# Optimization experiments

Measured on AMD Instinct MI355X. Metric: run time of the kernel, lower is better.

## Reference

```python
import jax, jax.numpy as jnp
import numpy as np

N, H, L, O = 8192, 512, 3, 512
LN_EPS = 1e-5


def setup_inputs() -> dict:
    key = jax.random.key(0)
    ks = jax.random.split(key, 8)
    # sparse symmetric adjacency with positive weights, zero diagonal
    u = jax.random.uniform(ks[0], (N, N))
    w = jax.random.uniform(ks[1], (N, N)) * 0.9 + 0.1
    A = jnp.where(u < 0.004, w, 0.0)
    A = (A + A.T) * 0.5
    A = A * (1.0 - jnp.eye(N, dtype=A.dtype))
    s = 0.02
    return {
        "node_feat": jax.random.normal(ks[2], (1, N, H), jnp.float32),
        "adj": A[None],
        "conv_w": jax.random.normal(ks[3], (L, H, H), jnp.float32) * s,
        "conv_b": jnp.zeros((L, H), jnp.float32),
        "mlp_w": jax.random.normal(ks[4], (L, H, H), jnp.float32) * s,
        "mlp_b": jnp.zeros((L, H), jnp.float32),
        "ln_g": jnp.ones((L, H), jnp.float32),
        "ln_b": jnp.zeros((L, H), jnp.float32),
        "lin_w": jax.random.normal(ks[5], (H, O), jnp.float32) * s,
        "lin_b": jnp.zeros((O,), jnp.float32),
    }


def _layer_norm(x, g, b):
    mu = jnp.mean(x, axis=-1, keepdims=True)
    var = jnp.mean(jnp.square(x - mu), axis=-1, keepdims=True)
    return (x - mu) * jax.lax.rsqrt(var + LN_EPS) * g + b


def reference(node_feat, adj, conv_w, conv_b, mlp_w, mlp_b, ln_g, ln_b, lin_w, lin_b):
    x = node_feat[0]          # [N, H]
    A = adj[0]                # [N, N]
    A = jnp.where(A > 0, A, 0.0)  # edges are positive entries only
    # gcn_norm: add self-loops (weight 1) only where missing
    d = jnp.diagonal(A)
    A1 = A + jnp.diag(jnp.where(d > 0, 0.0, 1.0))
    # deg scattered at target (edge_index[1] = column)
    deg = jnp.sum(A1, axis=0)
    dinv = jnp.where(deg > 0, deg ** -0.5, 0.0)
    Ahat = dinv[:, None] * A1 * dinv[None, :]  # [N, N]
    for l in range(L):
        # GCNConv: linear, propagate (aggregate at col), bias
        x = Ahat.T @ (x @ conv_w[l]) + conv_b[l]
        # MLP: Linear -> LayerNorm -> ReLU
        x = jax.nn.relu(_layer_norm(x @ mlp_w[l] + mlp_b[l], ln_g[l], ln_b[l]))
    mu = (x @ lin_w + lin_b)[None]  # [1, N, O]
    return mu
```

## Files before the change

### kernel.cpp

```cpp
#include <hip/hip_runtime.h>

#define NN 8192
#define HD 512
#define NL 3
#define CAPQ 48
#define CAPR (4 * CAPQ)
#define NWB (273 * NL)
#define NSB 2048
#define LN_EPS 1e-5f

typedef _Float16 f16;
typedef _Float16 f16x8 __attribute__((ext_vector_type(8)));
typedef _Float16 f16x4 __attribute__((ext_vector_type(4)));
typedef _Float16 f16x2 __attribute__((ext_vector_type(2)));
typedef float f32x4 __attribute__((ext_vector_type(4)));

__device__ __forceinline__ unsigned short f16_bits(f16 h) {
  union { f16 h; unsigned short u; } x; x.h = h; return x.u;
}
__device__ __forceinline__ f16 bits_f16(unsigned short u) {
  union { unsigned short u; f16 h; } x; x.u = u; return x.h;
}

__global__ __launch_bounds__(256) void k_prep(const float* __restrict__ A,
                                              const float* __restrict__ convw,
                                              const float* __restrict__ mlpw,
                                              const float* __restrict__ convb,
                                              const float* __restrict__ mlpb,
                                              const float* __restrict__ lw,
                                              unsigned* __restrict__ ell,
                                              int* __restrict__ nnz8q,
                                              float* __restrict__ psum,
                                              f16* __restrict__ WlT,
                                              float* __restrict__ bl,
                                              f16* __restrict__ lwT) {
  const int b = blockIdx.x;
  const int t = threadIdx.x;

  if (b < NWB) {
    const int l = b / 273;
    const int bx = b % 273;
    if (bx < 256) {
      const int m0 = bx * 2;
      const float* Wc = convw + (size_t)l * HD * HD;
      const float* Wm = mlpw + (size_t)l * HD * HD;
      f16* o = WlT + (size_t)l * HD * HD;
      float a00 = 0.f, a01 = 0.f, a10 = 0.f, a11 = 0.f;
      const float* wc0 = Wc + (size_t)m0 * HD;
      const float* wc1 = Wc + (size_t)(m0 + 1) * HD;
      for (int k = 0; k < HD; k++) {
        const float w0 = Wm[(size_t)k * HD + t];
        const float w1 = Wm[(size_t)k * HD + t + 256];
        const float c0 = wc0[k];
        const float c1 = wc1[k];
        a00 = fmaf(c0, w0, a00);
        a01 = fmaf(c0, w1, a01);
        a10 = fmaf(c1, w0, a10);
        a11 = fmaf(c1, w1, a11);
      }
      o[(size_t)t * HD + m0] = (f16)a00;
      o[(size_t)(t + 256) * HD + m0] = (f16)a01;
      o[(size_t)t * HD + m0 + 1] = (f16)a10;
      o[(size_t)(t + 256) * HD + m0 + 1] = (f16)a11;
    } else if (bx == 256) {
      const float* Wm = mlpw + (size_t)l * HD * HD;
      float acc0 = mlpb[l * HD + t];
      float acc1 = mlpb[l * HD + t + 256];
      for (int k = 0; k < HD; k++) {
        const float cb = convb[l * HD + k];
        acc0 = fmaf(cb, Wm[(size_t)k * HD + t], acc0);
        acc1 = fmaf(cb, Wm[(size_t)k * HD + t + 256], acc1);
      }
      bl[l * HD + t] = acc0;
      bl[l * HD + t + 256] = acc1;
    } else if (l == 0) {
      const int base = (bx - 257) * 16384;
      #pragma unroll 4
      for (int j = 0; j < 64; j++) {
        const int idx = base + j * 256 + t;
        const int k = idx >> 9, n = idx & 511;
        lwT[(size_t)n * HD + k] = (f16)lw[idx];
      }
    }
    return;
  }

  const int lane = t & 63;
  const int wid = (b - NWB) * 4 + (t >> 6);

  auto LOADQ = [&](int qidx, float4* v) {
    const int r = qidx >> 2, seg = qidx & 3;
    const float4* aseg = (const float4*)(A + (size_t)r * NN + seg * 2048);
    #pragma unroll
    for (int i = 0; i < 8; i++) v[i] = aseg[lane + i * 64];
  };

  auto PROC = [&](int qidx, const float4* v) {
    const int r = qidx >> 2, seg = qidx & 3;
    unsigned* er = ell + (size_t)qidx * CAPQ;
    int c = 0;
    float s = 0.f;
    #pragma unroll
    for (int i = 0; i < 8; i++) {
      c += (v[i].x > 0.f) + (v[i].y > 0.f) + (v[i].z > 0.f) + (v[i].w > 0.f);
      s += v[i].x + v[i].y + v[i].z + v[i].w;
    }
    int inc = c;
    #pragma unroll
    for (int d = 1; d < 64; d <<= 1) {
      int vv = __shfl_up(inc, d);
      if (lane >= d) inc += vv;
    }
    float ss = s;
    #pragma unroll
    for (int m = 1; m < 64; m <<= 1) ss += __shfl_xor(ss, m);
    int o = inc - c;
    #pragma unroll
    for (int i = 0; i < 8; i++) {
      const int cb = seg * 2048 + (lane + i * 64) * 4;
      float vals[4] = {v[i].x, v[i].y, v[i].z, v[i].w};
      #pragma unroll
      for (int q = 0; q < 4; q++) {
        if (vals[q] > 0.f) {
          if (o < CAPQ) er[o] = ((unsigned)f16_bits((f16)vals[q]) << 16) | (unsigned)(cb + q);
          o++;
        }
      }
    }
    int ne = __shfl(inc, 63);
    if (lane == 0) {
      if (ne > CAPQ) ne = CAPQ;
      const bool own = (seg == (r >> 11));
      if (own && ne < CAPQ) { er[ne] = (0x3C00u << 16) | (unsigned)r; ne++; }
      const int n8 = (ne + 7) & ~7;
      for (int k = ne; k < n8; k++) er[k] = (unsigned)r;
      nnz8q[qidx] = n8;
      psum[qidx] = ss;
    }
  };

  float4 va[8], vb[8];
  LOADQ(wid, va);
  LOADQ(wid + 8192, vb);
  PROC(wid, va);
  LOADQ(wid + 16384, va);
  PROC(wid + 8192, vb);
  LOADQ(wid + 24576, vb);
  PROC(wid + 16384, va);
  PROC(wid + 24576, vb);
}

__global__ __launch_bounds__(256) void k_deg(const float* __restrict__ psum,
                                             const float* __restrict__ x0,
                                             float* __restrict__ dinv,
                                             f16* __restrict__ xs) {
  const int r = blockIdx.x * 4 + (threadIdx.x >> 6);
  const int lane = threadIdx.x & 63;
  const float4 ps = *(const float4*)(psum + (size_t)r * 4);
  const float di = rsqrtf(ps.x + ps.y + ps.z + ps.w + 1.f);
  if (lane == 0) dinv[r] = di;
  const float4* xr = (const float4*)(x0 + (size_t)r * HD);
  const float4 a = xr[lane * 2];
  const float4 bq = xr[lane * 2 + 1];
  f16x8 o = {(f16)(a.x * di), (f16)(a.y * di), (f16)(a.z * di), (f16)(a.w * di),
             (f16)(bq.x * di), (f16)(bq.y * di), (f16)(bq.z * di), (f16)(bq.w * di)};
  *(f16x8*)(xs + (size_t)r * HD + lane * 8) = o;
}

__global__ __launch_bounds__(256) void k_spmm(const unsigned* __restrict__ ell,
                                              const int* __restrict__ nnz8q,
                                              const float* __restrict__ dinv,
                                              const f16* __restrict__ xs,
                                              f16* __restrict__ y) {
  const int bid = blockIdx.x;
  const int chunk = bid & 3;
  const int rb = bid >> 2;
  const int r = __builtin_amdgcn_readfirstlane(rb * 4 + (threadIdx.x >> 6));
  const int lane = threadIdx.x & 63;
  const int c0 = chunk * 128 + lane * 2;
  const unsigned* erow = ell + (size_t)r * CAPR;
  const int4 nn = *(const int4*)(nnz8q + (size_t)r * 4);
  const int ne8s[4] = {nn.x >> 3, nn.y >> 3, nn.z >> 3, nn.w >> 3};
  const f16* xc = xs + c0;
  float a0 = 0.f, a1 = 0.f;
  #pragma unroll
  for (int seg = 0; seg < 4; seg++) {
    const uint4* er = (const uint4*)(erow + seg * CAPQ);
    const int ne8 = ne8s[seg];
    for (int e8 = 0; e8 < ne8; e8++) {
      const uint4 ea = er[e8 * 2];
      const uint4 eb = er[e8 * 2 + 1];
      unsigned wv[8] = {ea.x, ea.y, ea.z, ea.w, eb.x, eb.y, eb.z, eb.w};
      f16x2 xv[8];
      #pragma unroll
      for (int q = 0; q < 8; q++)
        xv[q] = *(const f16x2*)(xc + (size_t)(wv[q] & 0xFFFFu) * HD);
      #pragma unroll
      for (int q = 0; q < 8; q++) {
        const float fw = (float)bits_f16((unsigned short)(wv[q] >> 16));
        a0 = fmaf(fw, (float)xv[q][0], a0);
        a1 = fmaf(fw, (float)xv[q][1], a1);
      }
    }
  }
  const float s = dinv[r];
  f16x2 o = {(f16)(a0 * s), (f16)(a1 * s)};
  *(f16x2*)(y + (size_t)r * HD + c0) = o;
}

__global__ __launch_bounds__(512) void k_gemm_ln(const f16* __restrict__ y,
                                                 const f16* __restrict__ WT,
                                                 const float* __restrict__ bias,
                                                 const float* __restrict__ g,
                                                 const float* __restrict__ bb,
                                                 const float* __restrict__ dscale,
                                                 f16* __restrict__ outp) {
  __shared__ float red[32][4][2];
  const int t = threadIdx.x;
  const int lane = t & 63;
  const int w = t >> 6;
  const int wm = w >> 2;
  const int wn = w & 3;
  const int m0 = blockIdx.x * 32;
  const int rl = lane & 15, kg = (lane >> 4) * 8;
  const f16* aP = y + (size_t)(m0 + wm * 16 + rl) * HD + kg;
  const f16* bP = WT + (size_t)(wn * 128 + rl) * HD + kg;

  f32x4 acc[8];
  #pragma unroll
  for (int j = 0; j < 8; j++) { f32x4 z = {0.f, 0.f, 0.f, 0.f}; acc[j] = z; }

  #pragma unroll 2
  for (int ks = 0; ks < HD; ks += 32) {
    const f16x8 af = *(const f16x8*)(aP + ks);
    #pragma unroll
    for (int j = 0; j < 8; j++) {
      const f16x8 bf = *(const f16x8*)(bP + (size_t)j * 16 * HD + ks);
      acc[j] = __builtin_amdgcn_mfma_f32_16x16x32_f16(af, bf, acc[j], 0, 0, 0);
    }
  }

  const int cg = lane >> 4, cl = lane & 15;
  float av[8][4];
  #pragma unroll
  for (int j = 0; j < 8; j++) {
    const float bv = bias[wn * 128 + j * 16 + cl];
    #pragma unroll
    for (int r = 0; r < 4; r++) av[j][r] = acc[j][r] + bv;
  }
  #pragma unroll
  for (int r = 0; r < 4; r++) {
    float s = 0.f, sq = 0.f;
    #pragma unroll
    for (int j = 0; j < 8; j++) { s += av[j][r]; sq += av[j][r] * av[j][r]; }
    #pragma unroll
    for (int m = 1; m < 16; m <<= 1) { s += __shfl_xor(s, m); sq += __shfl_xor(sq, m); }
    if (cl == 0) {
      red[wm * 16 + cg * 4 + r][wn][0] = s;
      red[wm * 16 + cg * 4 + r][wn][1] = sq;
    }
  }
  __syncthreads();
  #pragma unroll
  for (int r = 0; r < 4; r++) {
    const int rb = wm * 16 + cg * 4 + r;
    float s = 0.f, sq = 0.f;
    #pragma unroll
    for (int q = 0; q < 4; q++) { s += red[rb][q][0]; sq += red[rb][q][1]; }
    const float mu = s * (1.f / HD);
    const float rs = rsqrtf(sq * (1.f / HD) - mu * mu + LN_EPS);
    const int row = m0 + rb;
    const float dsc = dscale ? dscale[row] : 1.f;
    #pragma unroll
    for (int j = 0; j < 8; j++) {
      const int col = wn * 128 + j * 16 + cl;
      const float val = fmaxf((av[j][r] - mu) * rs * g[col] + bb[col], 0.f) * dsc;
      outp[(size_t)row * HD + col] = (f16)val;
    }
  }
}

__global__ __launch_bounds__(256) void k_gemm_direct(const f16* __restrict__ A,
                                                     const f16* __restrict__ BT,
                                                     float* __restrict__ C,
                                                     const float* __restrict__ bias) {
  const int t = threadIdx.x;
  const int lane = t & 63;
  const int wave = t >> 6;
  const int wm = wave >> 1, wn = wave & 1;
  const int m0 = blockIdx.x * 128, n0 = blockIdx.y * 128;
  const int rl = lane & 15, kg = (lane >> 4) * 8;

  const f16* aP[4];
  const f16* bP[4];
  #pragma unroll
  for (int i = 0; i < 4; i++)
    aP[i] = A + (size_t)(m0 + wm * 64 + i * 16 + rl) * HD + kg;
  #pragma unroll
  for (int j = 0; j < 4; j++)
    bP[j] = BT + (size_t)(n0 + wn * 64 + j * 16 + rl) * HD + kg;

  f32x4 acc[4][4];
  #pragma unroll
  for (int i = 0; i < 4; i++)
    #pragma unroll
    for (int j = 0; j < 4; j++) {
      f32x4 z = {0.f, 0.f, 0.f, 0.f};
      acc[i][j] = z;
    }

  #pragma unroll 4
  for (int ks = 0; ks < HD; ks += 32) {
    f16x8 af[4], bf[4];
    #pragma unroll
    for (int i = 0; i < 4; i++) af[i] = *(const f16x8*)(aP[i] + ks);
    #pragma unroll
    for (int j = 0; j < 4; j++) bf[j] = *(const f16x8*)(bP[j] + ks);
    #pragma unroll
    for (int i = 0; i < 4; i++)
      #pragma unroll
      for (int j = 0; j < 4; j++)
        acc[i][j] = __builtin_amdgcn_mfma_f32_16x16x32_f16(af[i], bf[j], acc[i][j], 0, 0, 0);
  }

  const int cg = lane >> 4, cl = lane & 15;
  #pragma unroll
  for (int i = 0; i < 4; i++) {
    #pragma unroll
    for (int j = 0; j < 4; j++) {
      const int col = n0 + wn * 64 + j * 16 + cl;
      const float bv = bias ? bias[col] : 0.f;
      #pragma unroll
      for (int rr = 0; rr < 4; rr++) {
        const int row = m0 + wm * 64 + i * 16 + cg * 4 + rr;
        C[(size_t)row * HD + col] = acc[i][j][rr] + bv;
      }
    }
  }
}

extern "C" void kernel_launch(void* const* d_in, const int* in_sizes, int n_in,
                              void* d_out, int out_size, void* d_ws, size_t ws_size,
                              hipStream_t stream) {
  const float* node_feat = (const float*)d_in[0];
  const float* adj       = (const float*)d_in[1];
  const float* conv_w    = (const float*)d_in[2];
  const float* conv_b    = (const float*)d_in[3];
  const float* mlp_w     = (const float*)d_in[4];
  const float* mlp_b     = (const float*)d_in[5];
  const float* ln_g      = (const float*)d_in[6];
  const float* ln_b      = (const float*)d_in[7];
  const float* lin_w     = (const float*)d_in[8];
  const float* lin_b     = (const float*)d_in[9];
  float* out = (float*)d_out;

  char* p = (char*)d_ws;
  unsigned* ell = (unsigned*)p; p += (size_t)NN * CAPR * 4;
  int* nnz8q = (int*)p;  p += (size_t)NN * 4 * 4;
  float* psum = (float*)p; p += (size_t)NN * 4 * 4;
  float* dinv = (float*)p; p += (size_t)NN * 4;
  f16* xsA   = (f16*)p;   p += (size_t)NN * HD * 2;
  f16* xsB   = (f16*)p;   p += (size_t)NN * HD * 2;
  f16* ybuf  = (f16*)p;   p += (size_t)NN * HD * 2;
  f16* WlT   = (f16*)p;   p += (size_t)NL * HD * HD * 2;
  f16* lwT   = (f16*)p;   p += (size_t)HD * HD * 2;
  float* bl  = (float*)p; p += (size_t)NL * HD * 4;

  k_prep<<<NWB + NSB, 256, 0, stream>>>(adj, conv_w, mlp_w, conv_b, mlp_b,
                                        lin_w, ell, nnz8q, psum, WlT, bl, lwT);
  k_deg<<<NN / 4, 256, 0, stream>>>(psum, node_feat, dinv, xsA);

  f16* xcur = xsA;
  for (int l = 0; l < NL; l++) {
    k_spmm<<<NN, 256, 0, stream>>>(ell, nnz8q, dinv, xcur, ybuf);
    f16* nxt = (xcur == xsA) ? xsB : xsA;
    k_gemm_ln<<<NN / 32, 512, 0, stream>>>(ybuf, WlT + (size_t)l * HD * HD,
                                           bl + l * HD, ln_g + l * HD, ln_b + l * HD,
                                           (l < 2) ? dinv : nullptr, nxt);
    xcur = nxt;
  }
  k_gemm_direct<<<dim3(64, 4), 256, 0, stream>>>(xcur, lwT, out, lin_b);
}
```

Before: 330.7 us.

## Stage ELL segments in LDS and write coalesced, one quarter-row per wave

The adjacency-to-ELL conversion now gives each wave exactly one quarter-row segment, launching many more blocks instead of looping four segments per wave with register double-buffering. Nonzeros are compacted into a shared-memory stage buffer pre-filled with the padding index and then written to global memory with one coalesced store per lane, replacing scattered per-element global writes and the serial padding loop. The per-segment capacity rises from 48 to 64 so each lane stores exactly one slot, which writes more ELL bytes and gives up the explicit load/process overlap in exchange for simpler, coalesced stores.

```diff
diff --git a/kernel.cpp b/kernel.cpp
--- a/kernel.cpp
+++ b/kernel.cpp
@@ -3,10 +3,9 @@
 #define NN 8192
 #define HD 512
 #define NL 3
-#define CAPQ 48
+#define CAPQ 64
 #define CAPR (4 * CAPQ)
 #define NWB (273 * NL)
-#define NSB 2048
 #define LN_EPS 1e-5f
 
 typedef _Float16 f16;
@@ -85,69 +84,60 @@
     return;
   }
 
+  __shared__ unsigned stage[4][CAPQ];
   const int lane = t & 63;
-  const int wid = (b - NWB) * 4 + (t >> 6);
-
-  auto LOADQ = [&](int qidx, float4* v) {
-    const int r = qidx >> 2, seg = qidx & 3;
-    const float4* aseg = (const float4*)(A + (size_t)r * NN + seg * 2048);
-    #pragma unroll
-    for (int i = 0; i < 8; i++) v[i] = aseg[lane + i * 64];
-  };
-
-  auto PROC = [&](int qidx, const float4* v) {
-    const int r = qidx >> 2, seg = qidx & 3;
-    unsigned* er = ell + (size_t)qidx * CAPQ;
-    int c = 0;
-    float s = 0.f;
-    #pragma unroll
-    for (int i = 0; i < 8; i++) {
-      c += (v[i].x > 0.f) + (v[i].y > 0.f) + (v[i].z > 0.f) + (v[i].w > 0.f);
-      s += v[i].x + v[i].y + v[i].z + v[i].w;
-    }
-    int inc = c;
-    #pragma unroll
-    for (int d = 1; d < 64; d <<= 1) {
-      int vv = __shfl_up(inc, d);
-      if (lane >= d) inc += vv;
-    }
-    float ss = s;
-    #pragma unroll
-    for (int m = 1; m < 64; m <<= 1) ss += __shfl_xor(ss, m);
-    int o = inc - c;
-    #pragma unroll
-    for (int i = 0; i < 8; i++) {
-      const int cb = seg * 2048 + (lane + i * 64) * 4;
-      float vals[4] = {v[i].x, v[i].y, v[i].z, v[i].w};
-      #pragma unroll
-      for (int q = 0; q < 4; q++) {
-        if (vals[q] > 0.f) {
-          if (o < CAPQ) er[o] = ((unsigned)f16_bits((f16)vals[q]) << 16) | (unsigned)(cb + q);
-          o++;
-        }
-      }
-    }
-    int ne = __shfl(inc, 63);
-    if (lane == 0) {
-      if (ne > CAPQ) ne = CAPQ;
-      const bool own = (seg == (r >> 11));
-      if (own && ne < CAPQ) { er[ne] = (0x3C00u << 16) | (unsigned)r; ne++; }
-      const int n8 = (ne + 7) & ~7;
-      for (int k = ne; k < n8; k++) er[k] = (unsigned)r;
-      nnz8q[qidx] = n8;
-      psum[qidx] = ss;
-    }
-  };
-
-  float4 va[8], vb[8];
-  LOADQ(wid, va);
-  LOADQ(wid + 8192, vb);
-  PROC(wid, va);
-  LOADQ(wid + 16384, va);
-  PROC(wid + 8192, vb);
-  LOADQ(wid + 24576, vb);
-  PROC(wid + 16384, va);
-  PROC(wid + 24576, vb);
+  const int w = t >> 6;
+  const int qidx = (b - NWB) * 4 + w;
+  const int r = qidx >> 2, seg = qidx & 3;
+  const float4* aseg = (const float4*)(A + (size_t)r * NN + seg * 2048);
+  unsigned* er = ell + (size_t)qidx * CAPQ;
+  unsigned* st = stage[w];
+
+  st[lane] = (unsigned)r;
+
+  float4 v[8];
+  #pragma unroll
+  for (int i = 0; i < 8; i++) v[i] = aseg[lane + i * 64];
+
+  int c = 0;
+  float s = 0.f;
+  #pragma unroll
+  for (int i = 0; i < 8; i++) {
+    c += (v[i].x > 0.f) + (v[i].y > 0.f) + (v[i].z > 0.f) + (v[i].w > 0.f);
+    s += v[i].x + v[i].y + v[i].z + v[i].w;
+  }
+  int inc = c;
+  #pragma unroll
+  for (int d = 1; d < 64; d <<= 1) {
+    int vv = __shfl_up(inc, d);
+    if (lane >= d) inc += vv;
+  }
+  float ss = s;
+  #pragma unroll
+  for (int m = 1; m < 64; m <<= 1) ss += __shfl_xor(ss, m);
+
+  int o = inc - c;
+  #pragma unroll
+  for (int i = 0; i < 8; i++) {
+    const int cb = seg * 2048 + (lane + i * 64) * 4;
+    float vals[4] = {v[i].x, v[i].y, v[i].z, v[i].w};
+    #pragma unroll
+    for (int q = 0; q < 4; q++) {
+      if (vals[q] > 0.f) {
+        if (o < CAPQ) st[o] = ((unsigned)f16_bits((f16)vals[q]) << 16) | (unsigned)(cb + q);
+        o++;
+      }
+    }
+  }
+  if (lane == 63) {
+    int ne = inc;
+    if (ne > CAPQ) ne = CAPQ;
+    const bool own = (seg == (r >> 11));
+    if (own && ne < CAPQ) { st[ne] = (0x3C00u << 16) | (unsigned)r; ne++; }
+    nnz8q[qidx] = (ne + 7) & ~7;
+    psum[qidx] = ss;
+  }
+  er[lane] = st[lane];
 }
 
 __global__ __launch_bounds__(256) void k_deg(const float* __restrict__ psum,
@@ -366,8 +356,8 @@
   f16* lwT   = (f16*)p;   p += (size_t)HD * HD * 2;
   float* bl  = (float*)p; p += (size_t)NL * HD * 4;
 
-  k_prep<<<NWB + NSB, 256, 0, stream>>>(adj, conv_w, mlp_w, conv_b, mlp_b,
-                                        lin_w, ell, nnz8q, psum, WlT, bl, lwT);
+  k_prep<<<NWB + NN, 256, 0, stream>>>(adj, conv_w, mlp_w, conv_b, mlp_b,
+                                       lin_w, ell, nnz8q, psum, WlT, bl, lwT);
   k_deg<<<NN / 4, 256, 0, stream>>>(psum, node_feat, dinv, xsA);
 
   f16* xcur = xsA;
```

Result: no change. 330.7 us (+0.0%).
